# Kernel tuning notes

Measured on AMD Instinct MI355X. Metric: run time of the kernel, lower is better.

Reference implementation:

```python
import jax, jax.numpy as jnp
import numpy as np

N, C, H, W = 32, 1, 512, 1024
SAMPLE_NUM = 5000
SIGMA = 0.03
ALPHA = 1.0
EPS = 1e-6
LOSS_WEIGHT = 1.0


def setup_inputs() -> dict:
    key = jax.random.key(0)
    k0, k1, k2, k3 = jax.random.split(key, 4)
    prediction = jax.random.normal(k0, (N, C, H, W), dtype=jnp.float32)
    # depths strictly > 0 so target > mask_value (=-1e-8) holds for every pixel,
    # matching the common case where all pixels are 'effective'.
    target = jax.random.uniform(k1, (N, C, H, W), dtype=jnp.float32,
                                minval=0.1, maxval=10.0)
    mask = jax.random.randint(k2, (N, C, H, W), 0, 2).astype(bool)
    # per-image random permutation of pixel indices -> disjoint pairs (A, B),
    # reproducing torch.randperm-based pair sampling as constant indices.
    perm = jax.vmap(lambda k: jax.random.permutation(k, H * W))(
        jax.random.split(k3, N))                      # [N, H*W] int32
    idx_A = perm[:, 0:2 * SAMPLE_NUM:2]               # [N, S]
    idx_B = perm[:, 1:2 * SAMPLE_NUM:2]               # [N, S]
    return {"prediction": prediction, "target": target, "mask": mask,
            "idx_A": idx_A, "idx_B": idx_B}


def reference(prediction, target, mask, idx_A, idx_B):
    n = target.shape[0]
    p = prediction.reshape(n, -1)   # [N, H*W]
    t = target.reshape(n, -1)
    m = mask.reshape(n, -1)

    iA = jnp.take_along_axis(p, idx_A, axis=1)   # [N, S]
    iB = jnp.take_along_axis(p, idx_B, axis=1)
    tA = jnp.take_along_axis(t, idx_A, axis=1)
    tB = jnp.take_along_axis(t, idx_B, axis=1)
    mA = jnp.take_along_axis(m, idx_A, axis=1)
    mB = jnpp_take(m, idx_B) if False else jnp.take_along_axis(m, idx_B, axis=1)

    ratio = tA / (tB + EPS)
    hi = 1.0 + SIGMA
    lo = 1.0 / (1.0 + SIGMA)
    mask_eq = (ratio < hi) & (ratio > lo)
    labels = jnp.where(ratio >= hi, 1.0,
                       jnp.where(ratio <= lo, -1.0, 0.0)).astype(p.dtype)
    cmask = mA & mB

    eq_sel = mask_eq & cmask
    uneq_sel = (~mask_eq) & cmask

    equal_loss = jnp.where(eq_sel, (iA - iB) ** 2, 0.0).sum()
    unequal_loss = jnp.where(
        uneq_sel, jnp.log1p(jnp.exp((iB - iA) * labels)), 0.0).sum()
    valid_samples = cmask.sum().astype(p.dtype)

    loss = (ALPHA * equal_loss + unequal_loss) / (valid_samples + EPS)
    return loss * LOSS_WEIGHT
```

## Files before the change

### kernel.cpp

```cpp
#include <hip/hip_runtime.h>
#include <math.h>

#define SAMPLE_NUM 5000
#define HWSZ (512 * 1024)
#define SIGMA_F 0.03f
#define EPS_F 1e-6f
#define BLOCK 256
#define NTOT 32
#define PACK_WORDS16 (NTOT * HWSZ / 16)


__global__ void __launch_bounds__(BLOCK)
mask_pack(const void* __restrict__ mask_raw,
          unsigned short* __restrict__ out) {
  const unsigned int* mw = (const unsigned int*)mask_raw;
  bool mask_is_i32 = true;
  #pragma unroll
  for (int w = 0; w < 32; ++w) {
    if (mw[w] > 1u) mask_is_i32 = false;
  }

  const int i = blockIdx.x * BLOCK + threadIdx.x;
  if (i >= PACK_WORDS16) return;

  unsigned short r;
  if (mask_is_i32) {
    const int* m32 = (const int*)mask_raw;
    const int b = i * 16;
    unsigned v = 0;
    #pragma unroll
    for (int k = 0; k < 16; ++k) v |= (unsigned)(m32[b + k] & 1) << k;
    r = (unsigned short)v;
  } else {
    const uint4 v = ((const uint4*)mask_raw)[i];
    const unsigned n0 = ((v.x & 0x01010101u) * 0x01020408u) >> 24;
    const unsigned n1 = ((v.y & 0x01010101u) * 0x01020408u) >> 24;
    const unsigned n2 = ((v.z & 0x01010101u) * 0x01020408u) >> 24;
    const unsigned n3 = ((v.w & 0x01010101u) * 0x01020408u) >> 24;
    r = (unsigned short)((n0 & 0xFu) | ((n1 & 0xFu) << 4) |
                         ((n2 & 0xFu) << 8) | ((n3 & 0xFu) << 12));
  }
  out[i] = r;
}

__global__ void __launch_bounds__(BLOCK)
ranking_loss_partial(const float* __restrict__ pred,
                     const float* __restrict__ targ,
                     const unsigned int* __restrict__ mpacked,
                     const int* __restrict__ idxA,
                     const int* __restrict__ idxB,
                     float* __restrict__ ws, int total) {
  const float hi = 1.0f + SIGMA_F;
  const float lo = 1.0f / (1.0f + SIGMA_F);

  float eq_sum = 0.0f, uneq_sum = 0.0f, valid = 0.0f;
  const int i = blockIdx.x * BLOCK + threadIdx.x;
  if (i < total) {
    const int n = i / SAMPLE_NUM;
    const int base = n * HWSZ;
    const int a = idxA[i];
    const int b = idxB[i];
    const int ia_off = base + a;
    const int ib_off = base + b;

    const unsigned wa = mpacked[ia_off >> 5];
    const unsigned wb = mpacked[ib_off >> 5];

    if ((wa >> (ia_off & 31)) & (wb >> (ib_off & 31)) & 1u) {
      const float tA = targ[ia_off];
      const float tB = targ[ib_off];
      const float iA = pred[ia_off];
      const float iB = pred[ib_off];

      valid += 1.0f;
      const float ratio = tA / (tB + EPS_F);
      if (ratio < hi && ratio > lo) {
        const float d = iA - iB;
        eq_sum += d * d;
      } else {
        const float label = (ratio >= hi) ? 1.0f : -1.0f;
        const float x = (iB - iA) * label;
        uneq_sum += (x > 20.0f) ? x : log1pf(expf(x));
      }
    }
  }

  #pragma unroll
  for (int off = 32; off > 0; off >>= 1) {
    eq_sum   += __shfl_down(eq_sum, off, 64);
    uneq_sum += __shfl_down(uneq_sum, off, 64);
    valid    += __shfl_down(valid, off, 64);
  }

  __shared__ float s_eq[4], s_un[4], s_va[4];
  const int lane = threadIdx.x & 63;
  const int wave = threadIdx.x >> 6;
  if (lane == 0) {
    s_eq[wave] = eq_sum;
    s_un[wave] = uneq_sum;
    s_va[wave] = valid;
  }
  __syncthreads();

  if (threadIdx.x == 0) {
    float e = 0.0f, u = 0.0f, v = 0.0f;
    #pragma unroll
    for (int w = 0; w < BLOCK / 64; ++w) {
      e += s_eq[w];
      u += s_un[w];
      v += s_va[w];
    }
    float* slot = ws + 3 * blockIdx.x;
    slot[0] = e;
    slot[1] = u;
    slot[2] = v;
  }
}

__global__ void __launch_bounds__(BLOCK)
ranking_loss_finalize(const float* __restrict__ ws, float* __restrict__ out,
                      int nblocks) {
  float e = 0.0f, u = 0.0f, v = 0.0f;
  for (int s = threadIdx.x; s < nblocks; s += BLOCK) {
    e += ws[3 * s + 0];
    u += ws[3 * s + 1];
    v += ws[3 * s + 2];
  }
  #pragma unroll
  for (int off = 32; off > 0; off >>= 1) {
    e += __shfl_down(e, off, 64);
    u += __shfl_down(u, off, 64);
    v += __shfl_down(v, off, 64);
  }
  __shared__ float s_e[4], s_u[4], s_v[4];
  const int lane = threadIdx.x & 63;
  const int wave = threadIdx.x >> 6;
  if (lane == 0) {
    s_e[wave] = e;
    s_u[wave] = u;
    s_v[wave] = v;
  }
  __syncthreads();
  if (threadIdx.x == 0) {
    float te = 0.0f, tu = 0.0f, tv = 0.0f;
    #pragma unroll
    for (int w = 0; w < BLOCK / 64; ++w) {
      te += s_e[w];
      tu += s_u[w];
      tv += s_v[w];
    }
    out[0] = (te + tu) / (tv + EPS_F);
  }
}

extern "C" void kernel_launch(void* const* d_in, const int* in_sizes, int n_in,
                              void* d_out, int out_size, void* d_ws,
                              size_t ws_size, hipStream_t stream) {
  const float* pred = (const float*)d_in[0];
  const float* targ = (const float*)d_in[1];
  const void* mask = d_in[2];
  const int* idxA = (const int*)d_in[3];
  const int* idxB = (const int*)d_in[4];
  float* out = (float*)d_out;
  float* ws = (float*)d_ws;

  const int total = in_sizes[3];
  const int grid = (total + BLOCK - 1) / BLOCK;

  unsigned short* mpack16 = (unsigned short*)((char*)d_ws + 8192);
  const unsigned int* mpack32 = (const unsigned int*)mpack16;

  mask_pack<<<PACK_WORDS16 / BLOCK, BLOCK, 0, stream>>>(mask, mpack16);
  ranking_loss_partial<<<grid, BLOCK, 0, stream>>>(pred, targ, mpack32, idxA,
                                                   idxB, ws, total);
  ranking_loss_finalize<<<1, BLOCK, 0, stream>>>(ws, out, grid);
}
```

Before: 178.6 us.

## Fuse mask packing with pair validity check into per-image LDS kernel

Replaces the grid-wide mask packing kernel with one block per image that packs the image's mask into a shared-memory bitmap and immediately evaluates pair validity for all sampled index pairs, emitting a compact per-pair ballot bitmap. The partial-loss kernel then reads one bit per pair instead of gathering two bits from a global packed mask. This removes the global packed-mask write and the scattered mask gathers. In exchange, the first kernel runs only one block per image, which limits parallelism while streaming the full mask.

```diff
diff --git a/kernel.cpp b/kernel.cpp
--- a/kernel.cpp
+++ b/kernel.cpp
@@ -6,13 +6,33 @@
 #define SIGMA_F 0.03f
 #define EPS_F 1e-6f
 #define BLOCK 256
-#define NTOT 32
-#define PACK_WORDS16 (NTOT * HWSZ / 16)
-
-
-__global__ void __launch_bounds__(BLOCK)
-mask_pack(const void* __restrict__ mask_raw,
-          unsigned short* __restrict__ out) {
+#define K1_THREADS 512
+#define ROW_BITS_PAD 5120
+#define BM_OFF_BYTES 8192
+
+
+__device__ __forceinline__ unsigned pack16_bytes(uint4 v) {
+  const unsigned n0 = ((v.x & 0x01010101u) * 0x01020408u) >> 24;
+  const unsigned n1 = ((v.y & 0x01010101u) * 0x01020408u) >> 24;
+  const unsigned n2 = ((v.z & 0x01010101u) * 0x01020408u) >> 24;
+  const unsigned n3 = ((v.w & 0x01010101u) * 0x01020408u) >> 24;
+  return (n0 & 0xFu) | ((n1 & 0xFu) << 4) | ((n2 & 0xFu) << 8) |
+         ((n3 & 0xFu) << 12);
+}
+
+__device__ __forceinline__ unsigned lsb4_i32(uint4 v) {
+  return (v.x & 1u) | ((v.y & 1u) << 1) | ((v.z & 1u) << 2) |
+         ((v.w & 1u) << 3);
+}
+
+__global__ void __launch_bounds__(K1_THREADS)
+mask_validity(const void* __restrict__ mask_raw,
+              const int* __restrict__ idxA, const int* __restrict__ idxB,
+              unsigned long long* __restrict__ bitmap) {
+  extern __shared__ unsigned int sbm[];
+  const int n = blockIdx.x;
+  const int t = threadIdx.x;
+
   const unsigned int* mw = (const unsigned int*)mask_raw;
   bool mask_is_i32 = true;
   #pragma unroll
@@ -20,33 +40,62 @@
     if (mw[w] > 1u) mask_is_i32 = false;
   }
 
-  const int i = blockIdx.x * BLOCK + threadIdx.x;
-  if (i >= PACK_WORDS16) return;
-
-  unsigned short r;
-  if (mask_is_i32) {
-    const int* m32 = (const int*)mask_raw;
-    const int b = i * 16;
-    unsigned v = 0;
+  unsigned short* sbm16 = (unsigned short*)sbm;
+  if (!mask_is_i32) {
+    const uint4* src =
+        (const uint4*)((const unsigned char*)mask_raw + (size_t)n * HWSZ);
     #pragma unroll
-    for (int k = 0; k < 16; ++k) v |= (unsigned)(m32[b + k] & 1) << k;
-    r = (unsigned short)v;
+    for (int it = 0; it < 16; ++it) {
+      const int c0 = t + (it * 4 + 0) * K1_THREADS;
+      const int c1 = t + (it * 4 + 1) * K1_THREADS;
+      const int c2 = t + (it * 4 + 2) * K1_THREADS;
+      const int c3 = t + (it * 4 + 3) * K1_THREADS;
+      const uint4 v0 = src[c0];
+      const uint4 v1 = src[c1];
+      const uint4 v2 = src[c2];
+      const uint4 v3 = src[c3];
+      sbm16[c0] = (unsigned short)pack16_bytes(v0);
+      sbm16[c1] = (unsigned short)pack16_bytes(v1);
+      sbm16[c2] = (unsigned short)pack16_bytes(v2);
+      sbm16[c3] = (unsigned short)pack16_bytes(v3);
+    }
   } else {
-    const uint4 v = ((const uint4*)mask_raw)[i];
-    const unsigned n0 = ((v.x & 0x01010101u) * 0x01020408u) >> 24;
-    const unsigned n1 = ((v.y & 0x01010101u) * 0x01020408u) >> 24;
-    const unsigned n2 = ((v.z & 0x01010101u) * 0x01020408u) >> 24;
-    const unsigned n3 = ((v.w & 0x01010101u) * 0x01020408u) >> 24;
-    r = (unsigned short)((n0 & 0xFu) | ((n1 & 0xFu) << 4) |
-                         ((n2 & 0xFu) << 8) | ((n3 & 0xFu) << 12));
-  }
-  out[i] = r;
+    const uint4* src =
+        (const uint4*)((const int*)mask_raw + (size_t)n * HWSZ);
+    for (int it = 0; it < 64; ++it) {
+      const int g = t + it * K1_THREADS;
+      const uint4 a = src[4 * g + 0];
+      const uint4 b = src[4 * g + 1];
+      const uint4 c = src[4 * g + 2];
+      const uint4 d = src[4 * g + 3];
+      sbm16[g] = (unsigned short)(lsb4_i32(a) | (lsb4_i32(b) << 4) |
+                                  (lsb4_i32(c) << 8) | (lsb4_i32(d) << 12));
+    }
+  }
+  __syncthreads();
+
+  const int lane = t & 63;
+  const int wv = t >> 6;
+  #pragma unroll
+  for (int j = 0; j < 10; ++j) {
+    const int il = wv * 64 + lane + j * K1_THREADS;
+    bool valid = false;
+    if (il < SAMPLE_NUM) {
+      const int i = n * SAMPLE_NUM + il;
+      const int a = idxA[i];
+      const int b = idxB[i];
+      valid =
+          ((sbm[a >> 5] >> (a & 31)) & (sbm[b >> 5] >> (b & 31)) & 1u) != 0u;
+    }
+    const unsigned long long bal = __ballot(valid);
+    if (lane == 0) bitmap[n * (ROW_BITS_PAD / 64) + (wv + j * 8)] = bal;
+  }
 }
 
 __global__ void __launch_bounds__(BLOCK)
 ranking_loss_partial(const float* __restrict__ pred,
                      const float* __restrict__ targ,
-                     const unsigned int* __restrict__ mpacked,
+                     const unsigned int* __restrict__ bitmap32,
                      const int* __restrict__ idxA,
                      const int* __restrict__ idxB,
                      float* __restrict__ ws, int total) {
@@ -57,30 +106,29 @@
   const int i = blockIdx.x * BLOCK + threadIdx.x;
   if (i < total) {
     const int n = i / SAMPLE_NUM;
-    const int base = n * HWSZ;
+    const int il = i - n * SAMPLE_NUM;
+    const unsigned w = bitmap32[n * (ROW_BITS_PAD / 32) + (il >> 5)];
     const int a = idxA[i];
     const int b = idxB[i];
-    const int ia_off = base + a;
-    const int ib_off = base + b;
-
-    const unsigned wa = mpacked[ia_off >> 5];
-    const unsigned wb = mpacked[ib_off >> 5];
-
-    if ((wa >> (ia_off & 31)) & (wb >> (ib_off & 31)) & 1u) {
+
+    if ((w >> (il & 31)) & 1u) {
+      const int base = n * HWSZ;
+      const int ia_off = base + a;
+      const int ib_off = base + b;
       const float tA = targ[ia_off];
       const float tB = targ[ib_off];
       const float iA = pred[ia_off];
       const float iB = pred[ib_off];
 
-      valid += 1.0f;
+      valid = 1.0f;
       const float ratio = tA / (tB + EPS_F);
       if (ratio < hi && ratio > lo) {
         const float d = iA - iB;
-        eq_sum += d * d;
+        eq_sum = d * d;
       } else {
         const float label = (ratio >= hi) ? 1.0f : -1.0f;
         const float x = (iB - iA) * label;
-        uneq_sum += (x > 20.0f) ? x : log1pf(expf(x));
+        uneq_sum = (x > 20.0f) ? x : log1pf(expf(x));
       }
     }
   }
@@ -105,10 +153,10 @@
   if (threadIdx.x == 0) {
     float e = 0.0f, u = 0.0f, v = 0.0f;
     #pragma unroll
-    for (int w = 0; w < BLOCK / 64; ++w) {
-      e += s_eq[w];
-      u += s_un[w];
-      v += s_va[w];
+    for (int w2 = 0; w2 < BLOCK / 64; ++w2) {
+      e += s_eq[w2];
+      u += s_un[w2];
+      v += s_va[w2];
     }
     float* slot = ws + 3 * blockIdx.x;
     slot[0] = e;
@@ -165,13 +213,16 @@
   float* ws = (float*)d_ws;
 
   const int total = in_sizes[3];
+  const int rows = total / SAMPLE_NUM;
   const int grid = (total + BLOCK - 1) / BLOCK;
 
-  unsigned short* mpack16 = (unsigned short*)((char*)d_ws + 8192);
-  const unsigned int* mpack32 = (const unsigned int*)mpack16;
-
-  mask_pack<<<PACK_WORDS16 / BLOCK, BLOCK, 0, stream>>>(mask, mpack16);
-  ranking_loss_partial<<<grid, BLOCK, 0, stream>>>(pred, targ, mpack32, idxA,
+  unsigned long long* bm64 =
+      (unsigned long long*)((char*)d_ws + BM_OFF_BYTES);
+  const unsigned int* bm32 = (const unsigned int*)bm64;
+
+  mask_validity<<<rows, K1_THREADS, HWSZ / 8, stream>>>(mask, idxA, idxB,
+                                                        bm64);
+  ranking_loss_partial<<<grid, BLOCK, 0, stream>>>(pred, targ, bm32, idxA,
                                                    idxB, ws, total);
   ranking_loss_finalize<<<1, BLOCK, 0, stream>>>(ws, out, grid);
 }
```

Result: slower. 220.0 us (+23.2%).

## Precompute per-pair mask validity bitmap via LDS-staged packed mask

Applied to the files above, without the earlier changes.

Adds a kernel that stages each image's packed mask (64 KiB) into shared memory, evaluates the mask bit for both indices of every pair, and writes a per-pair validity bitmap using wave ballots. The main kernel then reads one coalesced bitmap word instead of two scattered packed-mask words before deciding whether to gather target and prediction values. This replaces random global reads with LDS reads, at the cost of an extra kernel launch, 32 blocks each loading a full mask row, and a second read of idxA and idxB.

```diff
diff --git a/kernel.cpp b/kernel.cpp
--- a/kernel.cpp
+++ b/kernel.cpp
@@ -8,6 +8,9 @@
 #define BLOCK 256
 #define NTOT 32
 #define PACK_WORDS16 (NTOT * HWSZ / 16)
+#define ROW_BITS_PAD 5120
+#define BM_OFF_BYTES 8192
+#define PK_OFF_BYTES 32768
 
 
 __global__ void __launch_bounds__(BLOCK)
@@ -43,10 +46,44 @@
   out[i] = r;
 }
 
+__global__ void __launch_bounds__(1024)
+mask_validity(const unsigned int* __restrict__ mpack32,
+              const int* __restrict__ idxA, const int* __restrict__ idxB,
+              unsigned long long* __restrict__ bitmap) {
+  extern __shared__ unsigned int sbm[];
+  const int n = blockIdx.x;
+  const int t = threadIdx.x;
+
+  const uint4* src = (const uint4*)(mpack32 + n * (HWSZ / 32));
+  uint4* dst = (uint4*)sbm;
+  #pragma unroll
+  for (int it = 0; it < 4; ++it) {
+    dst[t + it * 1024] = src[t + it * 1024];
+  }
+  __syncthreads();
+
+  const int lane = t & 63;
+  const int wv = t >> 6;
+  #pragma unroll
+  for (int j = 0; j < 5; ++j) {
+    const int il = wv * 64 + lane + j * 1024;
+    bool valid = false;
+    if (il < SAMPLE_NUM) {
+      const int i = n * SAMPLE_NUM + il;
+      const int a = idxA[i];
+      const int b = idxB[i];
+      valid =
+          ((sbm[a >> 5] >> (a & 31)) & (sbm[b >> 5] >> (b & 31)) & 1u) != 0u;
+    }
+    const unsigned long long bal = __ballot(valid);
+    if (lane == 0) bitmap[n * (ROW_BITS_PAD / 64) + (wv + j * 16)] = bal;
+  }
+}
+
 __global__ void __launch_bounds__(BLOCK)
 ranking_loss_partial(const float* __restrict__ pred,
                      const float* __restrict__ targ,
-                     const unsigned int* __restrict__ mpacked,
+                     const unsigned int* __restrict__ bitmap32,
                      const int* __restrict__ idxA,
                      const int* __restrict__ idxB,
                      float* __restrict__ ws, int total) {
@@ -57,30 +94,29 @@
   const int i = blockIdx.x * BLOCK + threadIdx.x;
   if (i < total) {
     const int n = i / SAMPLE_NUM;
-    const int base = n * HWSZ;
+    const int il = i - n * SAMPLE_NUM;
+    const unsigned w = bitmap32[n * (ROW_BITS_PAD / 32) + (il >> 5)];
     const int a = idxA[i];
     const int b = idxB[i];
-    const int ia_off = base + a;
-    const int ib_off = base + b;
-
-    const unsigned wa = mpacked[ia_off >> 5];
-    const unsigned wb = mpacked[ib_off >> 5];
-
-    if ((wa >> (ia_off & 31)) & (wb >> (ib_off & 31)) & 1u) {
+
+    if ((w >> (il & 31)) & 1u) {
+      const int base = n * HWSZ;
+      const int ia_off = base + a;
+      const int ib_off = base + b;
       const float tA = targ[ia_off];
       const float tB = targ[ib_off];
       const float iA = pred[ia_off];
       const float iB = pred[ib_off];
 
-      valid += 1.0f;
+      valid = 1.0f;
       const float ratio = tA / (tB + EPS_F);
       if (ratio < hi && ratio > lo) {
         const float d = iA - iB;
-        eq_sum += d * d;
+        eq_sum = d * d;
       } else {
         const float label = (ratio >= hi) ? 1.0f : -1.0f;
         const float x = (iB - iA) * label;
-        uneq_sum += (x > 20.0f) ? x : log1pf(expf(x));
+        uneq_sum = (x > 20.0f) ? x : log1pf(expf(x));
       }
     }
   }
@@ -105,10 +141,10 @@
   if (threadIdx.x == 0) {
     float e = 0.0f, u = 0.0f, v = 0.0f;
     #pragma unroll
-    for (int w = 0; w < BLOCK / 64; ++w) {
-      e += s_eq[w];
-      u += s_un[w];
-      v += s_va[w];
+    for (int w2 = 0; w2 < BLOCK / 64; ++w2) {
+      e += s_eq[w2];
+      u += s_un[w2];
+      v += s_va[w2];
     }
     float* slot = ws + 3 * blockIdx.x;
     slot[0] = e;
@@ -165,13 +201,18 @@
   float* ws = (float*)d_ws;
 
   const int total = in_sizes[3];
+  const int rows = total / SAMPLE_NUM;
   const int grid = (total + BLOCK - 1) / BLOCK;
 
-  unsigned short* mpack16 = (unsigned short*)((char*)d_ws + 8192);
+  unsigned short* mpack16 = (unsigned short*)((char*)d_ws + PK_OFF_BYTES);
   const unsigned int* mpack32 = (const unsigned int*)mpack16;
+  unsigned long long* bm64 =
+      (unsigned long long*)((char*)d_ws + BM_OFF_BYTES);
+  const unsigned int* bm32 = (const unsigned int*)bm64;
 
   mask_pack<<<PACK_WORDS16 / BLOCK, BLOCK, 0, stream>>>(mask, mpack16);
-  ranking_loss_partial<<<grid, BLOCK, 0, stream>>>(pred, targ, mpack32, idxA,
+  mask_validity<<<rows, 1024, HWSZ / 8, stream>>>(mpack32, idxA, idxB, bm64);
+  ranking_loss_partial<<<grid, BLOCK, 0, stream>>>(pred, targ, bm32, idxA,
                                                    idxB, ws, total);
   ranking_loss_finalize<<<1, BLOCK, 0, stream>>>(ws, out, grid);
 }
```

Result: slower. 182.7 us (+2.3%).
